# Optimization experiments

Hardware: AMD Instinct MI355X
Metric: run time of the kernel (lower is better)

## Reference

```python
import jax, jax.numpy as jnp
import numpy as np

K = 512
DIM = 256
BETA = 0.25


def setup_inputs() -> dict:
    key = jax.random.key(0)
    k1, k2 = jax.random.split(key)
    x = jax.random.normal(k1, (64, DIM, 32, 32), dtype=jnp.float32)
    lookup_table = jax.random.normal(k2, (K, DIM), dtype=jnp.float32)
    return {"x": x, "lookup_table": lookup_table}


def reference(x, lookup_table):
    b, d, h, w = x.shape
    # [b,d,h,w] -> [b*h*w, d]
    xf = jnp.transpose(x, (0, 2, 3, 1)).reshape(-1, d)
    # Squared Euclidean distances (argmin identical to torch.cdist argmin)
    d2 = (
        jnp.sum(xf * xf, axis=-1, keepdims=True)
        - 2.0 * (xf @ lookup_table.T)
        + jnp.sum(lookup_table * lookup_table, axis=-1)
    )  # [N, K]
    q = jnp.argmin(d2, axis=1)  # [N]
    x_e = lookup_table[q].reshape(b, h, w, d).transpose(0, 3, 1, 2)  # [b,d,h,w]
    q_x = q.reshape(b, h, w)
    codebook_loss = jnp.mean(jnp.square(jax.lax.stop_gradient(x) - x_e))
    commitment_loss = jnp.mean(jnp.square(x - jax.lax.stop_gradient(x_e)))
    loss = codebook_loss + BETA * commitment_loss
    return x_e, q_x, loss
```

## Files before the change

### kernel.cpp

```cpp
#include <hip/hip_runtime.h>

#define DIM     256
#define HW      1024
#define N_ROWS  65536
#define NT      256
#define QBM     32
#define NBLK    2048
#define MARGIN  0.125f
#define MARGIN3 0.1875f

#define OUT_Q_OFF    16777216
#define OUT_LOSS_OFF 16842752

#define WS_DIST    512
#define WS_X2      2560
#define WS_CNTF_I  4608
#define WS_CNTP_I  4609
#define WS_LISTF_I 5120
#define WS_LISTP_I 21504
#define CAP_F      16384
#define CAP_P      32768
#define WS_LUTH_B  786432

#define VQ_LDS 49152

typedef _Float16 half8v __attribute__((ext_vector_type(8)));
typedef float floatx4 __attribute__((ext_vector_type(4)));

#define GLOAD_LDS16(gaddr, laddr) \
    __builtin_amdgcn_global_load_lds((const __attribute__((address_space(1))) unsigned int*)(gaddr), \
                                     (__attribute__((address_space(3))) unsigned int*)(laddr), 16, 0, 0)

__global__ void c2_kernel(const float* __restrict__ lut, float* __restrict__ ws) {
    if (threadIdx.x == 0) { ((int*)ws)[WS_CNTF_I] = 0; ((int*)ws)[WS_CNTP_I] = 0; }
    int t = threadIdx.x;
    for (int k = t; k < 512; k += 256) {
        const float4* row = (const float4*)(lut + (size_t)k * DIM);
        float s = 0.f;
        #pragma unroll 8
        for (int i = 0; i < DIM / 4; ++i) {
            float4 v = row[i];
            s += v.x * v.x + v.y * v.y + v.z * v.z + v.w * v.w;
        }
        ws[k] = s;
    }
}

__global__ void lutprep_kernel(const float* __restrict__ lut, float* __restrict__ ws) {
    int g = blockIdx.x * 256 + threadIdx.x;
    int lane = g & 63;
    int ctu  = (g >> 6) & 31;
    int dcg  = g >> 11;
    int code = ctu * 16 + (lane & 15);
    int d0   = dcg * 32 + (lane >> 4) * 8;
    const float* src = lut + (size_t)code * DIM + d0;
    half8v h;
    #pragma unroll
    for (int j = 0; j < 8; ++j) h[j] = (_Float16)src[j];
    char* dst = (char*)ws + WS_LUTH_B + (size_t)(dcg * 32 + ctu) * 1024 + lane * 16;
    *(half8v*)dst = h;
}

#define MERGE_TRIPLE(v1,i1,v2,i2,v3, w1,j1,w2,j2,w3)                          \
    {                                                                         \
        float a1,a2,a3,b1v,b2v; int a1i,a2i,b1i,b2i;                          \
        bool bf = (w1 < v1) || (w1 == v1 && j1 < i1);                         \
        if (bf) { a1=w1;a1i=j1;a2=w2;a2i=j2;a3=w3; b1v=v1;b1i=i1;b2v=v2;b2i=i2; } \
        else    { a1=v1;a1i=i1;a2=v2;a2i=i2;a3=v3; b1v=w1;b1i=j1;b2v=w2;b2i=j2; } \
        bool sa = (a2 < b1v) || (a2 == b1v && a2i < b1i);                     \
        v1 = a1; i1 = a1i;                                                    \
        if (sa) { v2 = a2; i2 = a2i; v3 = fminf(a3, b1v); }                   \
        else    { v2 = b1v; i2 = b1i; v3 = fminf(a2, b2v); }                  \
    }

__global__ __launch_bounds__(NT, 3) void vq_kernel(const float* __restrict__ x,
                                                   const float* __restrict__ lut,
                                                   float* __restrict__ out,
                                                   float* __restrict__ ws) {
    extern __shared__ char smem[];
    char* asmem = smem + 32768;
    const char* luth = (const char*)ws + WS_LUTH_B;

    const int tid = threadIdx.x;
    const int blk = blockIdx.x;
    const int n0  = blk * QBM;
    const int b   = n0 >> 10;
    const int hw0 = n0 & 1023;
    const float* xb = x + (size_t)b * (DIM * HW) + hw0;

    const int wave = tid >> 6;
    const int lane = tid & 63;
    const int l15  = lane & 15;
    const int l4   = lane >> 4;
    const int cg   = wave;

    float x2local = 0.f;
    {
        const int h = tid & 7;
        const int g = tid >> 3;
        const int dc = g >> 2, o = g & 3;
        float4 v[8];
        #pragma unroll
        for (int j = 0; j < 8; ++j)
            v[j] = *(const float4*)(xb + (size_t)(8 * g + j) * HW + 4 * h);
        #pragma unroll
        for (int j = 0; j < 8; ++j) {
            x2local = fmaf(v[j].x, v[j].x, x2local);
            x2local = fmaf(v[j].y, v[j].y, x2local);
            x2local = fmaf(v[j].z, v[j].z, x2local);
            x2local = fmaf(v[j].w, v[j].w, x2local);
        }
        #pragma unroll
        for (int r = 0; r < 4; ++r) {
            int row = 4 * h + r;
            half8v hh;
            #pragma unroll
            for (int j = 0; j < 8; ++j) {
                const float* vf = (const float*)&v[j];
                hh[j] = (_Float16)vf[r];
            }
            char* dst = asmem + (size_t)((row >> 4) * 8 + dc) * 1024 + (((row & 15) + 16 * o) * 16);
            *(half8v*)dst = hh;
        }
    }

    floatx4 acc[2][8];
    #pragma unroll
    for (int i = 0; i < 2; ++i)
        #pragma unroll
        for (int j = 0; j < 8; ++j) acc[i][j] = (floatx4)0.f;

    #pragma unroll
    for (int i = 0; i < 8; ++i) {
        int cc = wave * 8 + i;
        GLOAD_LDS16(luth + (size_t)(0 * 32 + cc) * 1024 + lane * 16, smem + cc * 1024);
    }
    __syncthreads();

    for (int dc = 0; dc < 8; ++dc) {
        asm volatile("s_waitcnt vmcnt(0)" ::: "memory");
        __builtin_amdgcn_sched_barrier(0);
        half8v ah[2], bh[8];
        #pragma unroll
        for (int rtl = 0; rtl < 2; ++rtl)
            ah[rtl] = *(const half8v*)(asmem + (size_t)(rtl * 8 + dc) * 1024 + lane * 16);
        #pragma unroll
        for (int ct = 0; ct < 8; ++ct)
            bh[ct] = *(const half8v*)(smem + (size_t)(cg * 8 + ct) * 1024 + lane * 16);
        asm volatile("s_waitcnt lgkmcnt(0)" ::: "memory");
        __builtin_amdgcn_sched_barrier(0);
        if (dc < 7) {
            #pragma unroll
            for (int i = 0; i < 8; ++i) {
                int cc = wave * 8 + i;
                GLOAD_LDS16(luth + (size_t)((dc + 1) * 32 + cc) * 1024 + lane * 16, smem + cc * 1024);
            }
        }
        #pragma unroll
        for (int ct = 0; ct < 8; ++ct)
            #pragma unroll
            for (int rtl = 0; rtl < 2; ++rtl)
                acc[rtl][ct] = __builtin_amdgcn_mfma_f32_16x16x32_f16(ah[rtl], bh[ct], acc[rtl][ct], 0, 0, 0);
    }
    __syncthreads();

    float* rv1   = (float*)smem;
    int*   ri1   = (int*)(smem + 512);
    float* rv2   = (float*)(smem + 1024);
    int*   ri2   = (int*)(smem + 1536);
    float* rv3   = (float*)(smem + 2048);
    int*   qsh   = (int*)(smem + 2560);
    float* wsumx = (float*)(smem + 2688);

    #pragma unroll
    for (int rt = 0; rt < 2; ++rt) {
        #pragma unroll
        for (int r = 0; r < 4; ++r) {
            float v1 = 3.4e38f, v2 = 3.4e38f, v3 = 3.4e38f; int i1 = 0, i2 = 0;
            #pragma unroll
            for (int ct = 0; ct < 8; ++ct) {
                int code = (cg * 8 + ct) * 16 + l15;
                float dist = fmaf(-2.f, acc[rt][ct][r], ws[code]);
                if (dist < v1)      { v3 = v2; v2 = v1; i2 = i1; v1 = dist; i1 = code; }
                else if (dist < v2) { v3 = v2; v2 = dist; i2 = code; }
                else if (dist < v3) { v3 = dist; }
            }
            #pragma unroll
            for (int off = 1; off < 16; off <<= 1) {
                float w1 = __shfl_xor(v1, off, 64);
                int   j1 = __shfl_xor(i1, off, 64);
                float w2 = __shfl_xor(v2, off, 64);
                int   j2 = __shfl_xor(i2, off, 64);
                float w3 = __shfl_xor(v3, off, 64);
                MERGE_TRIPLE(v1, i1, v2, i2, v3, w1, j1, w2, j2, w3);
            }
            if (l15 == 0) {
                int idx = cg * 32 + rt * 16 + l4 * 4 + r;
                rv1[idx] = v1; ri1[idx] = i1; rv2[idx] = v2; ri2[idx] = i2; rv3[idx] = v3;
            }
        }
    }
    __syncthreads();

    float dist_part = 0.f;
    if (tid < QBM) {
        const int row = tid;
        float m1 = rv1[row]; int n1 = ri1[row]; float m2 = rv2[row]; int n2 = ri2[row]; float m3 = rv3[row];
        #pragma unroll
        for (int s = 1; s < 4; ++s) {
            float w1 = rv1[s * 32 + row]; int j1 = ri1[s * 32 + row];
            float w2 = rv2[s * 32 + row]; int j2 = ri2[s * 32 + row];
            float w3 = rv3[s * 32 + row];
            MERGE_TRIPLE(m1, n1, m2, n2, m3, w1, j1, w2, j2, w3);
        }
        qsh[row] = n1;
        out[OUT_Q_OFF + n0 + row] = (float)n1;
        if (m2 - m1 <= MARGIN) {
            if (m3 - m1 > MARGIN3) {
                int idx = atomicAdd((int*)ws + WS_CNTP_I, 1);
                if (idx < CAP_P) {
                    ((int*)ws)[WS_LISTP_I + idx * 3 + 0] = n0 + row;
                    ((int*)ws)[WS_LISTP_I + idx * 3 + 1] = n1;
                    ((int*)ws)[WS_LISTP_I + idx * 3 + 2] = n2;
                }
            } else {
                int idx = atomicAdd((int*)ws + WS_CNTF_I, 1);
                if (idx < CAP_F) ((int*)ws)[WS_LISTF_I + idx] = n0 + row;
            }
        }
        dist_part = m1;
    }
    float dv = dist_part;
    #pragma unroll
    for (int off = 32; off; off >>= 1) dv += __shfl_down(dv, off, 64);
    if (tid == 0) ws[WS_DIST + blk] = dv;

    float xv = x2local;
    #pragma unroll
    for (int off = 32; off; off >>= 1) xv += __shfl_down(xv, off, 64);
    if (lane == 0) wsumx[wave] = xv;
    __syncthreads();
    if (tid == 0) ws[WS_X2 + blk] = wsumx[0] + wsumx[1] + wsumx[2] + wsumx[3];

    {
        const int h = tid & 7;
        const int g = tid >> 3;
        int qs[4];
        #pragma unroll
        for (int r = 0; r < 4; ++r) qs[r] = qsh[4 * h + r];
        float* ob = out + (size_t)b * (DIM * HW) + hw0 + 4 * h;
        #pragma unroll
        for (int j = 0; j < 8; ++j) {
            int d = 8 * g + j;
            float4 c;
            float* cp = (float*)&c;
            #pragma unroll
            for (int r = 0; r < 4; ++r) cp[r] = lut[(size_t)qs[r] * DIM + d];
            *(float4*)(ob + (size_t)d * HW) = c;
        }
    }
}

__global__ void recheck_kernel(const float* __restrict__ x, const float* __restrict__ lut,
                               float* __restrict__ out, const float* __restrict__ ws) {
    __shared__ float xrow[DIM];
    __shared__ float carow[DIM];
    __shared__ float cbrow[DIM];
    __shared__ float frv[256];
    __shared__ int   fri[256];
    __shared__ int   qq;
    const int tid = threadIdx.x;

    int cntp = ((const int*)ws)[WS_CNTP_I];
    if (cntp > CAP_P) cntp = CAP_P;
    const int* lp = (const int*)ws + WS_LISTP_I;
    for (int e = blockIdx.x; e < cntp; e += gridDim.x) {
        const int row = lp[e * 3 + 0];
        const int ia  = lp[e * 3 + 1];
        const int ib  = lp[e * 3 + 2];
        const int b = row >> 10, hw = row & 1023;
        xrow[tid]  = x[(size_t)b * (DIM * HW) + (size_t)tid * HW + hw];
        carow[tid] = lut[(size_t)ia * DIM + tid];
        cbrow[tid] = lut[(size_t)ib * DIM + tid];
        __syncthreads();
        if (tid == 0) {
            float dota = 0.f, dotb = 0.f;
            for (int d = 0; d < DIM; ++d) {
                dota = fmaf(xrow[d], carow[d], dota);
                dotb = fmaf(xrow[d], cbrow[d], dotb);
            }
            float da = fmaf(-2.f, dota, ws[ia]);
            float db = fmaf(-2.f, dotb, ws[ib]);
            int q;
            if (da < db) q = ia;
            else if (db < da) q = ib;
            else q = (ia < ib) ? ia : ib;
            qq = q;
            out[OUT_Q_OFF + row] = (float)q;
        }
        __syncthreads();
        const int q = qq;
        out[(size_t)b * (DIM * HW) + (size_t)tid * HW + hw] = lut[(size_t)q * DIM + tid];
        __syncthreads();
    }

    int cntf = ((const int*)ws)[WS_CNTF_I];
    if (cntf > CAP_F) cntf = CAP_F;
    const int* lf = (const int*)ws + WS_LISTF_I;
    for (int e = blockIdx.x; e < cntf; e += gridDim.x) {
        const int row = lf[e];
        const int b = row >> 10, hw = row & 1023;
        xrow[tid] = x[(size_t)b * (DIM * HW) + (size_t)tid * HW + hw];
        __syncthreads();
        float bv = 3.4e38f; int bi = 0;
        #pragma unroll
        for (int k2 = 0; k2 < 2; ++k2) {
            int k = tid + k2 * 256;
            const float* cr = lut + (size_t)k * DIM;
            float dot = 0.f;
            for (int d = 0; d < DIM; ++d) dot = fmaf(xrow[d], cr[d], dot);
            float dist = fmaf(-2.f, dot, ws[k]);
            if (dist < bv || (dist == bv && k < bi)) { bv = dist; bi = k; }
        }
        frv[tid] = bv; fri[tid] = bi;
        __syncthreads();
        for (int s = 128; s; s >>= 1) {
            if (tid < s) {
                float ov = frv[tid + s]; int oi = fri[tid + s];
                if (ov < frv[tid] || (ov == frv[tid] && oi < fri[tid])) {
                    frv[tid] = ov; fri[tid] = oi;
                }
            }
            __syncthreads();
        }
        const int q = fri[0];
        if (tid == 0) out[OUT_Q_OFF + row] = (float)q;
        out[(size_t)b * (DIM * HW) + (size_t)tid * HW + hw] = lut[(size_t)q * DIM + tid];
        __syncthreads();
    }
}

__global__ void loss_kernel(float* __restrict__ out, const float* __restrict__ ws) {
    __shared__ float wsum[4];
    int tid = threadIdx.x;
    float s = 0.f;
    for (int i = tid; i < 4096; i += 256) s += ws[WS_DIST + i];
    #pragma unroll
    for (int off = 32; off; off >>= 1) s += __shfl_down(s, off, 64);
    if ((tid & 63) == 0) wsum[tid >> 6] = s;
    __syncthreads();
    if (tid == 0) {
        float total = wsum[0] + wsum[1] + wsum[2] + wsum[3];
        out[OUT_LOSS_OFF] = total * (1.25f / 16777216.f);
    }
}

extern "C" void kernel_launch(void* const* d_in, const int* in_sizes, int n_in,
                              void* d_out, int out_size, void* d_ws, size_t ws_size,
                              hipStream_t stream) {
    const float* x   = (const float*)d_in[0];
    const float* lut = (const float*)d_in[1];
    float* out = (float*)d_out;
    float* ws  = (float*)d_ws;

    (void)hipFuncSetAttribute((const void*)vq_kernel,
                              hipFuncAttributeMaxDynamicSharedMemorySize, VQ_LDS);

    c2_kernel<<<1, 256, 0, stream>>>(lut, ws);
    lutprep_kernel<<<64, 256, 0, stream>>>(lut, ws);
    vq_kernel<<<NBLK, NT, VQ_LDS, stream>>>(x, lut, out, ws);
    recheck_kernel<<<2048, 256, 0, stream>>>(x, lut, out, ws);
    loss_kernel<<<1, 256, 0, stream>>>(out, ws);
}
```

Before: 126.3 us.

## Restructure VQ kernel to single-wave blocks with register-resident tiles and streamed codebook

After: 138.7 us. 1.1x slower.

```diff
diff --git a/kernel.cpp b/kernel.cpp
--- a/kernel.cpp
+++ b/kernel.cpp
@@ -3,7 +3,6 @@
 #define DIM     256
 #define HW      1024
 #define N_ROWS  65536
-#define NT      256
 #define QBM     32
 #define NBLK    2048
 #define MARGIN  0.125f
@@ -22,14 +21,8 @@
 #define CAP_P      32768
 #define WS_LUTH_B  786432
 
-#define VQ_LDS 49152
-
 typedef _Float16 half8v __attribute__((ext_vector_type(8)));
 typedef float floatx4 __attribute__((ext_vector_type(4)));
-
-#define GLOAD_LDS16(gaddr, laddr) \
-    __builtin_amdgcn_global_load_lds((const __attribute__((address_space(1))) unsigned int*)(gaddr), \
-                                     (__attribute__((address_space(3))) unsigned int*)(laddr), 16, 0, 0)
 
 __global__ void c2_kernel(const float* __restrict__ lut, float* __restrict__ ws) {
     if (threadIdx.x == 0) { ((int*)ws)[WS_CNTF_I] = 0; ((int*)ws)[WS_CNTP_I] = 0; }
@@ -73,190 +66,165 @@
         else    { v2 = b1v; i2 = b1i; v3 = fminf(a2, b2v); }                  \
     }
 
-__global__ __launch_bounds__(NT, 3) void vq_kernel(const float* __restrict__ x,
+#define CTU_BODY(CUR, NXT, CTU, DO_PREFETCH)                                          \
+    {                                                                                 \
+        if (DO_PREFETCH) {                                                            \
+            _Pragma("unroll")                                                         \
+            for (int dc = 0; dc < 8; ++dc)                                            \
+                NXT[dc] = *(const half8v*)(luth + (size_t)(dc * 32 + (CTU) + 1) * 1024 + lane * 16); \
+        }                                                                             \
+        floatx4 acc00 = (floatx4)0.f, acc01 = (floatx4)0.f;                           \
+        floatx4 acc10 = (floatx4)0.f, acc11 = (floatx4)0.f;                           \
+        _Pragma("unroll")                                                             \
+        for (int dc = 0; dc < 4; ++dc) {                                              \
+            acc00 = __builtin_amdgcn_mfma_f32_16x16x32_f16(a[0][dc], CUR[dc], acc00, 0, 0, 0); \
+            acc10 = __builtin_amdgcn_mfma_f32_16x16x32_f16(a[1][dc], CUR[dc], acc10, 0, 0, 0); \
+        }                                                                             \
+        _Pragma("unroll")                                                             \
+        for (int dc = 4; dc < 8; ++dc) {                                              \
+            acc01 = __builtin_amdgcn_mfma_f32_16x16x32_f16(a[0][dc], CUR[dc], acc01, 0, 0, 0); \
+            acc11 = __builtin_amdgcn_mfma_f32_16x16x32_f16(a[1][dc], CUR[dc], acc11, 0, 0, 0); \
+        }                                                                             \
+        float c2v = ws[(CTU) * 16 + l15];                                             \
+        int code = (CTU) * 16 + l15;                                                  \
+        _Pragma("unroll")                                                             \
+        for (int r = 0; r < 4; ++r) {                                                 \
+            float d0f = fmaf(-2.f, acc00[r] + acc01[r], c2v);                         \
+            if (d0f < v1[0][r])      { v3[0][r]=v2[0][r]; v2[0][r]=v1[0][r]; i2[0][r]=i1[0][r]; v1[0][r]=d0f; i1[0][r]=code; } \
+            else if (d0f < v2[0][r]) { v3[0][r]=v2[0][r]; v2[0][r]=d0f; i2[0][r]=code; } \
+            else if (d0f < v3[0][r]) { v3[0][r]=d0f; }                                \
+            float d1f = fmaf(-2.f, acc10[r] + acc11[r], c2v);                         \
+            if (d1f < v1[1][r])      { v3[1][r]=v2[1][r]; v2[1][r]=v1[1][r]; i2[1][r]=i1[1][r]; v1[1][r]=d1f; i1[1][r]=code; } \
+            else if (d1f < v2[1][r]) { v3[1][r]=v2[1][r]; v2[1][r]=d1f; i2[1][r]=code; } \
+            else if (d1f < v3[1][r]) { v3[1][r]=d1f; }                                \
+        }                                                                             \
+    }
+
+__global__ __launch_bounds__(64, 2) void vq_kernel(const float* __restrict__ x,
                                                    const float* __restrict__ lut,
                                                    float* __restrict__ out,
                                                    float* __restrict__ ws) {
-    extern __shared__ char smem[];
-    char* asmem = smem + 32768;
+    __shared__ int qsh[QBM];
     const char* luth = (const char*)ws + WS_LUTH_B;
 
-    const int tid = threadIdx.x;
-    const int blk = blockIdx.x;
-    const int n0  = blk * QBM;
-    const int b   = n0 >> 10;
-    const int hw0 = n0 & 1023;
+    const int lane = threadIdx.x;
+    const int blk  = blockIdx.x;
+    const int n0   = blk * QBM;
+    const int b    = n0 >> 10;
+    const int hw0  = n0 & 1023;
     const float* xb = x + (size_t)b * (DIM * HW) + hw0;
 
-    const int wave = tid >> 6;
-    const int lane = tid & 63;
-    const int l15  = lane & 15;
-    const int l4   = lane >> 4;
-    const int cg   = wave;
-
+    const int l15 = lane & 15;
+    const int l4  = lane >> 4;
+
+    half8v a[2][8];
     float x2local = 0.f;
-    {
-        const int h = tid & 7;
-        const int g = tid >> 3;
-        const int dc = g >> 2, o = g & 3;
-        float4 v[8];
-        #pragma unroll
-        for (int j = 0; j < 8; ++j)
-            v[j] = *(const float4*)(xb + (size_t)(8 * g + j) * HW + 4 * h);
-        #pragma unroll
-        for (int j = 0; j < 8; ++j) {
-            x2local = fmaf(v[j].x, v[j].x, x2local);
-            x2local = fmaf(v[j].y, v[j].y, x2local);
-            x2local = fmaf(v[j].z, v[j].z, x2local);
-            x2local = fmaf(v[j].w, v[j].w, x2local);
-        }
-        #pragma unroll
-        for (int r = 0; r < 4; ++r) {
-            int row = 4 * h + r;
+    #pragma unroll
+    for (int rt = 0; rt < 2; ++rt) {
+        #pragma unroll
+        for (int dc = 0; dc < 8; ++dc) {
+            const float* src = xb + (size_t)(dc * 32 + l4 * 8) * HW + rt * 16 + l15;
             half8v hh;
             #pragma unroll
             for (int j = 0; j < 8; ++j) {
-                const float* vf = (const float*)&v[j];
-                hh[j] = (_Float16)vf[r];
-            }
-            char* dst = asmem + (size_t)((row >> 4) * 8 + dc) * 1024 + (((row & 15) + 16 * o) * 16);
-            *(half8v*)dst = hh;
-        }
-    }
-
-    floatx4 acc[2][8];
-    #pragma unroll
-    for (int i = 0; i < 2; ++i)
-        #pragma unroll
-        for (int j = 0; j < 8; ++j) acc[i][j] = (floatx4)0.f;
-
-    #pragma unroll
-    for (int i = 0; i < 8; ++i) {
-        int cc = wave * 8 + i;
-        GLOAD_LDS16(luth + (size_t)(0 * 32 + cc) * 1024 + lane * 16, smem + cc * 1024);
-    }
-    __syncthreads();
-
-    for (int dc = 0; dc < 8; ++dc) {
-        asm volatile("s_waitcnt vmcnt(0)" ::: "memory");
-        __builtin_amdgcn_sched_barrier(0);
-        half8v ah[2], bh[8];
-        #pragma unroll
-        for (int rtl = 0; rtl < 2; ++rtl)
-            ah[rtl] = *(const half8v*)(asmem + (size_t)(rtl * 8 + dc) * 1024 + lane * 16);
-        #pragma unroll
-        for (int ct = 0; ct < 8; ++ct)
-            bh[ct] = *(const half8v*)(smem + (size_t)(cg * 8 + ct) * 1024 + lane * 16);
-        asm volatile("s_waitcnt lgkmcnt(0)" ::: "memory");
-        __builtin_amdgcn_sched_barrier(0);
-        if (dc < 7) {
-            #pragma unroll
-            for (int i = 0; i < 8; ++i) {
-                int cc = wave * 8 + i;
-                GLOAD_LDS16(luth + (size_t)((dc + 1) * 32 + cc) * 1024 + lane * 16, smem + cc * 1024);
-            }
-        }
-        #pragma unroll
-        for (int ct = 0; ct < 8; ++ct)
-            #pragma unroll
-            for (int rtl = 0; rtl < 2; ++rtl)
-                acc[rtl][ct] = __builtin_amdgcn_mfma_f32_16x16x32_f16(ah[rtl], bh[ct], acc[rtl][ct], 0, 0, 0);
-    }
-    __syncthreads();
-
-    float* rv1   = (float*)smem;
-    int*   ri1   = (int*)(smem + 512);
-    float* rv2   = (float*)(smem + 1024);
-    int*   ri2   = (int*)(smem + 1536);
-    float* rv3   = (float*)(smem + 2048);
-    int*   qsh   = (int*)(smem + 2560);
-    float* wsumx = (float*)(smem + 2688);
+                float v = src[(size_t)j * HW];
+                x2local = fmaf(v, v, x2local);
+                hh[j] = (_Float16)v;
+            }
+            a[rt][dc] = hh;
+        }
+    }
+
+    float v1[2][4], v2[2][4], v3[2][4]; int i1[2][4], i2[2][4];
+    #pragma unroll
+    for (int rt = 0; rt < 2; ++rt)
+        #pragma unroll
+        for (int r = 0; r < 4; ++r) { v1[rt][r]=3.4e38f; v2[rt][r]=3.4e38f; v3[rt][r]=3.4e38f; i1[rt][r]=0; i2[rt][r]=0; }
+
+    half8v bA[8], bB[8];
+    #pragma unroll
+    for (int dc = 0; dc < 8; ++dc)
+        bA[dc] = *(const half8v*)(luth + (size_t)(dc * 32 + 0) * 1024 + lane * 16);
+    for (int ctu2 = 0; ctu2 < 16; ++ctu2) {
+        const int ctuA = 2 * ctu2;
+        const int ctuB = 2 * ctu2 + 1;
+        CTU_BODY(bA, bB, ctuA, true);
+        CTU_BODY(bB, bA, ctuB, (ctu2 < 15));
+    }
 
     #pragma unroll
     for (int rt = 0; rt < 2; ++rt) {
         #pragma unroll
         for (int r = 0; r < 4; ++r) {
-            float v1 = 3.4e38f, v2 = 3.4e38f, v3 = 3.4e38f; int i1 = 0, i2 = 0;
-            #pragma unroll
-            for (int ct = 0; ct < 8; ++ct) {
-                int code = (cg * 8 + ct) * 16 + l15;
-                float dist = fmaf(-2.f, acc[rt][ct][r], ws[code]);
-                if (dist < v1)      { v3 = v2; v2 = v1; i2 = i1; v1 = dist; i1 = code; }
-                else if (dist < v2) { v3 = v2; v2 = dist; i2 = code; }
-                else if (dist < v3) { v3 = dist; }
-            }
             #pragma unroll
             for (int off = 1; off < 16; off <<= 1) {
-                float w1 = __shfl_xor(v1, off, 64);
-                int   j1 = __shfl_xor(i1, off, 64);
-                float w2 = __shfl_xor(v2, off, 64);
-                int   j2 = __shfl_xor(i2, off, 64);
-                float w3 = __shfl_xor(v3, off, 64);
-                MERGE_TRIPLE(v1, i1, v2, i2, v3, w1, j1, w2, j2, w3);
-            }
-            if (l15 == 0) {
-                int idx = cg * 32 + rt * 16 + l4 * 4 + r;
-                rv1[idx] = v1; ri1[idx] = i1; rv2[idx] = v2; ri2[idx] = i2; rv3[idx] = v3;
-            }
-        }
-    }
+                float w1 = __shfl_xor(v1[rt][r], off, 64);
+                int   j1 = __shfl_xor(i1[rt][r], off, 64);
+                float w2 = __shfl_xor(v2[rt][r], off, 64);
+                int   j2 = __shfl_xor(i2[rt][r], off, 64);
+                float w3 = __shfl_xor(v3[rt][r], off, 64);
+                MERGE_TRIPLE(v1[rt][r], i1[rt][r], v2[rt][r], i2[rt][r], v3[rt][r], w1, j1, w2, j2, w3);
+            }
+        }
+    }
+
+    float dist_part = 0.f;
+    if (l15 == 0) {
+        #pragma unroll
+        for (int rt = 0; rt < 2; ++rt) {
+            #pragma unroll
+            for (int r = 0; r < 4; ++r) {
+                int row = rt * 16 + l4 * 4 + r;
+                int n1 = i1[rt][r];
+                qsh[row] = n1;
+                out[OUT_Q_OFF + n0 + row] = (float)n1;
+                float m1 = v1[rt][r], m2 = v2[rt][r], m3 = v3[rt][r];
+                if (m2 - m1 <= MARGIN) {
+                    if (m3 - m1 > MARGIN3) {
+                        int idx = atomicAdd((int*)ws + WS_CNTP_I, 1);
+                        if (idx < CAP_P) {
+                            ((int*)ws)[WS_LISTP_I + idx * 3 + 0] = n0 + row;
+                            ((int*)ws)[WS_LISTP_I + idx * 3 + 1] = n1;
+                            ((int*)ws)[WS_LISTP_I + idx * 3 + 2] = i2[rt][r];
+                        }
+                    } else {
+                        int idx = atomicAdd((int*)ws + WS_CNTF_I, 1);
+                        if (idx < CAP_F) ((int*)ws)[WS_LISTF_I + idx] = n0 + row;
+                    }
+                }
+                dist_part += m1;
+            }
+        }
+    }
+    float dv = dist_part;
+    #pragma unroll
+    for (int off = 32; off; off >>= 1) dv += __shfl_down(dv, off, 64);
+    if (lane == 0) ws[WS_DIST + blk] = dv;
+    float xv = x2local;
+    #pragma unroll
+    for (int off = 32; off; off >>= 1) xv += __shfl_down(xv, off, 64);
+    if (lane == 0) ws[WS_X2 + blk] = xv;
+
     __syncthreads();
 
-    float dist_part = 0.f;
-    if (tid < QBM) {
-        const int row = tid;
-        float m1 = rv1[row]; int n1 = ri1[row]; float m2 = rv2[row]; int n2 = ri2[row]; float m3 = rv3[row];
-        #pragma unroll
-        for (int s = 1; s < 4; ++s) {
-            float w1 = rv1[s * 32 + row]; int j1 = ri1[s * 32 + row];
-            float w2 = rv2[s * 32 + row]; int j2 = ri2[s * 32 + row];
-            float w3 = rv3[s * 32 + row];
-            MERGE_TRIPLE(m1, n1, m2, n2, m3, w1, j1, w2, j2, w3);
-        }
-        qsh[row] = n1;
-        out[OUT_Q_OFF + n0 + row] = (float)n1;
-        if (m2 - m1 <= MARGIN) {
-            if (m3 - m1 > MARGIN3) {
-                int idx = atomicAdd((int*)ws + WS_CNTP_I, 1);
-                if (idx < CAP_P) {
-                    ((int*)ws)[WS_LISTP_I + idx * 3 + 0] = n0 + row;
-                    ((int*)ws)[WS_LISTP_I + idx * 3 + 1] = n1;
-                    ((int*)ws)[WS_LISTP_I + idx * 3 + 2] = n2;
-                }
-            } else {
-                int idx = atomicAdd((int*)ws + WS_CNTF_I, 1);
-                if (idx < CAP_F) ((int*)ws)[WS_LISTF_I + idx] = n0 + row;
-            }
-        }
-        dist_part = m1;
-    }
-    float dv = dist_part;
-    #pragma unroll
-    for (int off = 32; off; off >>= 1) dv += __shfl_down(dv, off, 64);
-    if (tid == 0) ws[WS_DIST + blk] = dv;
-
-    float xv = x2local;
-    #pragma unroll
-    for (int off = 32; off; off >>= 1) xv += __shfl_down(xv, off, 64);
-    if (lane == 0) wsumx[wave] = xv;
-    __syncthreads();
-    if (tid == 0) ws[WS_X2 + blk] = wsumx[0] + wsumx[1] + wsumx[2] + wsumx[3];
-
     {
-        const int h = tid & 7;
-        const int g = tid >> 3;
+        const int h = lane & 7;
+        const int g = lane >> 3;
         int qs[4];
         #pragma unroll
         for (int r = 0; r < 4; ++r) qs[r] = qsh[4 * h + r];
         float* ob = out + (size_t)b * (DIM * HW) + hw0 + 4 * h;
         #pragma unroll
-        for (int j = 0; j < 8; ++j) {
-            int d = 8 * g + j;
-            float4 c;
-            float* cp = (float*)&c;
+        for (int p = 0; p < 4; ++p) {
             #pragma unroll
-            for (int r = 0; r < 4; ++r) cp[r] = lut[(size_t)qs[r] * DIM + d];
-            *(float4*)(ob + (size_t)d * HW) = c;
+            for (int j = 0; j < 8; ++j) {
+                int d = (g + 8 * p) * 8 + j;
+                float4 c;
+                float* cp = (float*)&c;
+                #pragma unroll
+                for (int r = 0; r < 4; ++r) cp[r] = lut[(size_t)qs[r] * DIM + d];
+                *(float4*)(ob + (size_t)d * HW) = c;
+            }
         }
     }
 }
@@ -363,12 +331,9 @@
     float* out = (float*)d_out;
     float* ws  = (float*)d_ws;
 
-    (void)hipFuncSetAttribute((const void*)vq_kernel,
-                              hipFuncAttributeMaxDynamicSharedMemorySize, VQ_LDS);
-
     c2_kernel<<<1, 256, 0, stream>>>(lut, ws);
     lutprep_kernel<<<64, 256, 0, stream>>>(lut, ws);
-    vq_kernel<<<NBLK, NT, VQ_LDS, stream>>>(x, lut, out, ws);
+    vq_kernel<<<NBLK, 64, 0, stream>>>(x, lut, out, ws);
     recheck_kernel<<<2048, 256, 0, stream>>>(x, lut, out, ws);
     loss_kernel<<<1, 256, 0, stream>>>(out, ws);
 }
```
